# Optimization experiments

Measured on AMD Instinct MI355X. Metric: run time of the kernel, lower is better.

Reference implementation:

```python
import math
import jax, jax.numpy as jnp
import numpy as np

B, S, F, I, K, L, C = 2, 2048, 512, 1024, 3, 2, 256
BETA = 0.99                 # momentumnet_beta
INIT_SCALE = L ** -0.5      # per-cell output scale
PI = math.pi


def setup_inputs() -> dict:
    key = jax.random.key(0)
    ks = jax.random.split(key, 8)
    inp = jax.random.randint(ks[0], (B, S), 0, C)
    tgt = jax.random.randint(ks[1], (B, S), 0, C)
    emb = jax.random.normal(ks[2], (C, 2 * F), jnp.float32) * 0.02
    w0s = jax.random.normal(ks[3], (L, 3, I, F, 1), jnp.float32) * (F ** -0.5)
    w1s = jax.random.normal(ks[4], (L, 3, I, I, K), jnp.float32) * ((I * K) ** -0.5)
    w2s = jax.random.normal(ks[5], (L, 3, F, I, 1), jnp.float32) * (I ** -0.5)
    out_w = jax.random.normal(ks[6], (C, 2 * F, 1), jnp.float32) * ((2 * F) ** -0.5)
    out_b = jax.random.normal(ks[7], (C,), jnp.float32) * 0.02
    return {"inp": inp, "tgt": tgt, "emb": emb, "w0s": w0s, "w1s": w1s,
            "w2s": w2s, "out_w": out_w, "out_b": out_b}


def causal_conv(x, w):
    # x: [B, Cin, S], w: [Cout, Cin, k]; left-pad k-1 (matches torch pad+(k-1,0)+conv1d)
    k = w.shape[-1]
    return jax.lax.conv_general_dilated(x, w, (1,), [(k - 1, 0)],
                                        dimension_numbers=("NCH", "OIH", "NCH"))


def feed_forward(x, w0, w1, w2):
    x = jax.nn.relu(causal_conv(x, w0))
    x = jax.nn.relu(causal_conv(x, w1))
    return causal_conv(x, w2)


def norm(x):
    # mean-subtract + RMS-style L2 norm over channel dim (dim 1)
    x = x - x.mean(1, keepdims=True)
    return x / (jnp.linalg.norm(x, axis=1, keepdims=True) * (x.shape[1] ** -0.5) + 1e-5)


def _feature_embd():
    f = jnp.arange(F, dtype=jnp.float32)[:, None] + 1.0
    additive = f % 2.0
    f = (f - additive) / 2.0
    f = f * (8.0 / F) - math.log(C / (2.0 * PI))
    return jnp.exp(f) + additive * PI  # [F, 1]


def _forward(inp, tgt, emb, w0s, w1s, w2s, out_w, out_b):
    fe = _feature_embd()
    divisor = (jnp.arange(S, dtype=jnp.float32) + 1.0)[None, None, :]  # [1,1,S]
    x = emb[inp].transpose(0, 2, 1)         # [B, 2F, S]
    a, b = x[:, :F], x[:, F:]               # reversible streams [B, F, S]
    for l in range(L):
        h = b + fe                          # training-path positional embedding
        d = feed_forward(h, w0s[l, 0], w1s[l, 0], w2s[l, 0])
        sc = feed_forward(h, w0s[l, 1], w1s[l, 1], w2s[l, 1])
        sh = feed_forward(h, w0s[l, 2], w1s[l, 2], w2s[l, 2])
        cum = jnp.cumsum(d, axis=1)         # cumsum over feature dim (dim 1, as in source)
        cell = norm(cum / divisor * sc + sh) * INIT_SCALE
        c = BETA * a + (1.0 - BETA) * cell  # momentum coupling forward
        a, b = c, b + c                     # Identity layer with additive coupling
    streams = jnp.concatenate([a, b], axis=1)        # [B, 2F, S]
    logits = causal_conv(streams, out_w) + out_b[None, :, None]  # [B, C, S]
    logp = jax.nn.log_softmax(logits, axis=1)
    nll = -jnp.take_along_axis(logp, tgt[:, None, :], axis=1)[:, 0, :]
    return nll.mean()                       # torch cross_entropy (mean reduction)


def reference(inp, tgt, emb, w0s, w1s, w2s, out_w, out_b):
    return _forward(inp, tgt, emb, w0s, w1s, w2s, out_w, out_b)
```

## Files before the change

kernel.cpp:

```cpp
#include <hip/hip_runtime.h>

#define S_ 2048
#define F_ 512
#define I_ 1024
#define C_ 256

typedef float f4 __attribute__((ext_vector_type(4)));
typedef __bf16 bf8 __attribute__((ext_vector_type(8)));
typedef __bf16 bf4 __attribute__((ext_vector_type(4)));
typedef int i4v __attribute__((ext_vector_type(4)));
typedef int i8v __attribute__((ext_vector_type(8)));
typedef unsigned char u8;

__device__ __forceinline__ void gload_lds16(const void* g, void* l) {
  __builtin_amdgcn_global_load_lds(
      (const __attribute__((address_space(1))) void*)g,
      (__attribute__((address_space(3))) void*)l, 16, 0, 0);
}

__device__ __forceinline__ float fe_val(int f) {
  const float PI_F = 3.14159265358979323846f;
  float additive = (f & 1) ? 0.0f : 1.0f;
  float fv = ((float)(f + 1) - additive) * 0.5f;
  fv = fv * (8.0f / (float)F_) - logf((float)C_ / (2.0f * PI_F));
  return expf(fv) + additive * PI_F;
}

template <int KW, bool RELU, int OUT, int NTILE, int KD, int LDB>
__global__ __launch_bounds__(256) void gemm_f8(
    const u8* __restrict__ Ab, const u8* __restrict__ Bb, void* __restrict__ Cb,
    const u8* __restrict__ zpage, int M, int PZ, long sAp, long sBp, long sBb,
    long sCz) {
  constexpr int NF = NTILE / 32;
  constexpr int NIT = KD / 128;
  constexpr int AK = KW * KD;
  constexpr int BP = NTILE / 32;
  constexpr int NSTEP = KW * NIT;
  __shared__ u8 Asm[128 * 128];
  __shared__ u8 Bsm[NTILE * 128];
  const int tid = threadIdx.x;
  const int z = blockIdx.z;
  const int p = z % PZ;
  const int bb = z / PZ;
  const u8* A = Ab + (long)p * sAp;
  const u8* B = Bb + (long)bb * sBb + (long)p * sBp;
  const int m0 = blockIdx.y * 128;
  const int n0 = blockIdx.x * NTILE;
  const int lane = tid & 63;
  const int wave = tid >> 6;
  const int wr = wave >> 1;
  const int wc = wave & 1;
  const int l15 = lane & 15;
  const int quad = lane >> 4;
  const int cr = tid >> 3;
  const int csw = (((tid & 7) ^ (cr & 7)) << 4);
  const int off0 = (((2 * quad) ^ (l15 & 7)) << 4);
  const int off1 = (((2 * quad + 1) ^ (l15 & 7)) << 4);
  f4 acc[4][NF] = {};

  const int lin = blockIdx.x + gridDim.x * (blockIdx.y + gridDim.y * blockIdx.z);
  const int koff = ((lin >> 8) % 3) * (NSTEP / 3);

  auto kstep = [&](int ks) {
    const int t = (KW == 1) ? 0 : (ks / NIT);
    const int kb = (ks & (NIT - 1)) * 128;
    const u8* pA = A + (long)t * KD + kb;
#pragma unroll
    for (int g = 0; g < 4; ++g)
      gload_lds16(pA + (long)(m0 + g * 32 + cr) * AK + csw,
                  Asm + g * 4096 + wave * 1024);
#pragma unroll
    for (int g = 0; g < BP; ++g) {
      const int rg = n0 + g * 32 + cr + ((KW == 3) ? (t - 2) : 0);
      const u8* pB = (KW == 3 && rg < 0) ? (zpage + csw)
                                         : (B + (long)rg * LDB + kb + csw);
      gload_lds16(pB, Bsm + g * 4096 + wave * 1024);
    }
    __syncthreads();
    i8v af[4], bfr[NF];
#pragma unroll
    for (int mt = 0; mt < 4; ++mt) {
      const u8* rp = Asm + (wr * 64 + mt * 16 + l15) * 128;
      const i4v lo = *(const i4v*)(rp + off0);
      const i4v hi = *(const i4v*)(rp + off1);
      af[mt][0] = lo[0]; af[mt][1] = lo[1]; af[mt][2] = lo[2]; af[mt][3] = lo[3];
      af[mt][4] = hi[0]; af[mt][5] = hi[1]; af[mt][6] = hi[2]; af[mt][7] = hi[3];
    }
#pragma unroll
    for (int nt = 0; nt < NF; ++nt) {
      const u8* rp = Bsm + (wc * (NTILE / 2) + nt * 16 + l15) * 128;
      const i4v lo = *(const i4v*)(rp + off0);
      const i4v hi = *(const i4v*)(rp + off1);
      bfr[nt][0] = lo[0]; bfr[nt][1] = lo[1]; bfr[nt][2] = lo[2]; bfr[nt][3] = lo[3];
      bfr[nt][4] = hi[0]; bfr[nt][5] = hi[1]; bfr[nt][6] = hi[2]; bfr[nt][7] = hi[3];
    }
    __builtin_amdgcn_s_setprio(1);
#pragma unroll
    for (int mt = 0; mt < 4; ++mt)
#pragma unroll
      for (int nt = 0; nt < NF; ++nt)
        acc[mt][nt] = __builtin_amdgcn_mfma_scale_f32_16x16x128_f8f6f4(
            af[mt], bfr[nt], acc[mt][nt], 0, 0, 0, 0x7F7F7F7F, 0, 0x7F7F7F7F);
    __builtin_amdgcn_s_setprio(0);
    __syncthreads();
  };

#pragma unroll 1
  for (int ks = koff; ks < NSTEP; ++ks) kstep(ks);
#pragma unroll 1
  for (int ks = 0; ks < koff; ++ks) kstep(ks);

#pragma unroll
  for (int mt = 0; mt < 4; ++mt) {
    const int m = m0 + wr * 64 + mt * 16 + quad * 4;
#pragma unroll
    for (int nt = 0; nt < NF; ++nt) {
      const int n = n0 + wc * (NTILE / 2) + nt * 16 + l15;
      f4 v = acc[mt][nt];
#pragma unroll
      for (int q = 0; q < 4; ++q) {
        v[q] *= 0.015625f;
        if (RELU) v[q] = fmaxf(v[q], 0.0f);
      }
      if (OUT == 2) {
        int r = __builtin_amdgcn_cvt_pk_fp8_f32(v[0], v[1], 0, false);
        r = __builtin_amdgcn_cvt_pk_fp8_f32(v[2], v[3], r, true);
        *(int*)((u8*)Cb + (long)z * sCz + (long)n * M + m) = r;
      } else {
        *(f4*)((float*)Cb + (long)z * sCz + (long)n * M + m) = v;
      }
    }
  }
}

__device__ __forceinline__ void cvt4(const float* __restrict__ s,
                                     __bf16* __restrict__ d, long T) {
  const long i = T * 4;
  const float4 v = *(const float4*)(s + i);
  bf4 o;
  o[0] = (__bf16)v.x;
  o[1] = (__bf16)v.y;
  o[2] = (__bf16)v.z;
  o[3] = (__bf16)v.w;
  *(bf4*)(d + i) = o;
}

__device__ __forceinline__ void cvt4f8(const float* __restrict__ s,
                                       u8* __restrict__ d, long T) {
  const long i = T * 4;
  const float4 v = *(const float4*)(s + i);
  int r = __builtin_amdgcn_cvt_pk_fp8_f32(v.x * 64.0f, v.y * 64.0f, 0, false);
  r = __builtin_amdgcn_cvt_pk_fp8_f32(v.z * 64.0f, v.w * 64.0f, r, true);
  *(int*)(d + i) = r;
}

__device__ __forceinline__ int pk4f8(float a, float b, float c, float d) {
  int r = __builtin_amdgcn_cvt_pk_fp8_f32(a, b, 0, false);
  return __builtin_amdgcn_cvt_pk_fp8_f32(c, d, r, true);
}

__global__ void k_prep(const float* __restrict__ w0, const float* __restrict__ w2,
                       const float* __restrict__ ow, const float* __restrict__ w1,
                       u8* __restrict__ W0f8, u8* __restrict__ W2f8,
                       __bf16* __restrict__ OWc, u8* __restrict__ W1f8) {
  long T = (long)blockIdx.x * 256 + threadIdx.x;
  if (T < 786432L) {
    cvt4f8(w0, W0f8, T);
    return;
  }
  T -= 786432L;
  if (T < 786432L) {
    cvt4f8(w2, W2f8, T);
    return;
  }
  T -= 786432L;
  if (T < 65536L) {
    cvt4(ow, OWc, T);
    return;
  }
  T -= 65536L;
  const long j4 = T & 255;
  const long r3 = T >> 8;
  const float* src = w1 + r3 * 3072 + j4 * 12;
  const float4 v0 = *(const float4*)src;
  const float4 v1 = *(const float4*)(src + 4);
  const float4 v2 = *(const float4*)(src + 8);
  u8* dst = W1f8 + r3 * 3072 + j4 * 4;
  *(int*)(dst) = pk4f8(v0.x * 64.f, v0.w * 64.f, v1.z * 64.f, v2.y * 64.f);
  *(int*)(dst + 1024) = pk4f8(v0.y * 64.f, v1.x * 64.f, v1.w * 64.f, v2.z * 64.f);
  *(int*)(dst + 2048) = pk4f8(v0.z * 64.f, v1.y * 64.f, v2.x * 64.f, v2.w * 64.f);
}

__global__ __launch_bounds__(64) void k_embed(const int* __restrict__ inp,
                                              const float* __restrict__ emb,
                                              float* __restrict__ a_st,
                                              float* __restrict__ b_st,
                                              u8* __restrict__ h) {
  const int col = blockIdx.x;
  const int lane = threadIdx.x;
  const int f0 = lane * 8;
  const float* e = emb + (long)inp[col] * (2 * F_);
  const float4 a0 = *(const float4*)(e + f0);
  const float4 a1 = *(const float4*)(e + f0 + 4);
  const float4 b0 = *(const float4*)(e + F_ + f0);
  const float4 b1 = *(const float4*)(e + F_ + f0 + 4);
  *(float4*)(a_st + (long)col * F_ + f0) = a0;
  *(float4*)(a_st + (long)col * F_ + f0 + 4) = a1;
  *(float4*)(b_st + (long)col * F_ + f0) = b0;
  *(float4*)(b_st + (long)col * F_ + f0 + 4) = b1;
  const float bb[8] = {b0.x, b0.y, b0.z, b0.w, b1.x, b1.y, b1.z, b1.w};
  float hv[8];
#pragma unroll
  for (int q = 0; q < 8; ++q) hv[q] = bb[q] + fe_val(f0 + q);
  const int lo = pk4f8(hv[0], hv[1], hv[2], hv[3]);
  const int hi = pk4f8(hv[4], hv[5], hv[6], hv[7]);
  *(int2*)(h + (long)col * F_ + f0) = {lo, hi};
}

__global__ __launch_bounds__(64) void k_cell(const float* __restrict__ Y3,
                                             float* __restrict__ a_st,
                                             float* __restrict__ b_st,
                                             void* __restrict__ outp,
                                             int last) {
  const int col = blockIdx.x;
  const int s = col & (S_ - 1);
  const int b = col >> 11;
  const int lane = threadIdx.x;
  const int f0 = lane * 8;
  const float* d = Y3 + ((long)(3 * b + 0) * S_ + s) * F_ + f0;
  const float* sc = Y3 + ((long)(3 * b + 1) * S_ + s) * F_ + f0;
  const float* sh = Y3 + ((long)(3 * b + 2) * S_ + s) * F_ + f0;
  float* ap = a_st + (long)col * F_ + f0;
  float* bp = b_st + (long)col * F_ + f0;
  const float inv_div = 1.0f / (float)(s + 1);

  const float4 d0 = *(const float4*)d;
  const float4 d1 = *(const float4*)(d + 4);
  const float4 sc0 = *(const float4*)sc;
  const float4 sc1 = *(const float4*)(sc + 4);
  const float4 sh0 = *(const float4*)sh;
  const float4 sh1 = *(const float4*)(sh + 4);

  float c[8];
  c[0] = d0.x;
  c[1] = c[0] + d0.y;
  c[2] = c[1] + d0.z;
  c[3] = c[2] + d0.w;
  c[4] = c[3] + d1.x;
  c[5] = c[4] + d1.y;
  c[6] = c[5] + d1.z;
  c[7] = c[6] + d1.w;
  const float tot = c[7];
  float scan = tot;
#pragma unroll
  for (int off = 1; off < 64; off <<= 1) {
    float nb = __shfl_up(scan, off);
    if (lane >= off) scan += nb;
  }
  const float base = scan - tot;

  float v[8];
  v[0] = (base + c[0]) * inv_div * sc0.x + sh0.x;
  v[1] = (base + c[1]) * inv_div * sc0.y + sh0.y;
  v[2] = (base + c[2]) * inv_div * sc0.z + sh0.z;
  v[3] = (base + c[3]) * inv_div * sc0.w + sh0.w;
  v[4] = (base + c[4]) * inv_div * sc1.x + sh1.x;
  v[5] = (base + c[5]) * inv_div * sc1.y + sh1.y;
  v[6] = (base + c[6]) * inv_div * sc1.z + sh1.z;
  v[7] = (base + c[7]) * inv_div * sc1.w + sh1.w;

  float sum = 0.f, ssq = 0.f;
#pragma unroll
  for (int q = 0; q < 8; ++q) {
    sum += v[q];
    ssq += v[q] * v[q];
  }
#pragma unroll
  for (int off = 1; off < 64; off <<= 1) {
    sum += __shfl_xor(sum, off);
    ssq += __shfl_xor(ssq, off);
  }
  const float mean = sum * (1.0f / (float)F_);
  const float nsq = fmaxf(ssq - (float)F_ * mean * mean, 0.0f);
  const float denom = sqrtf(nsq) * 0.04419417382415922f + 1e-5f;
  const float isc = 0.7071067811865476f / denom;

  const float4 av0 = *(const float4*)ap;
  const float4 av1 = *(const float4*)(ap + 4);
  const float4 bv0 = *(const float4*)bp;
  const float4 bv1 = *(const float4*)(bp + 4);
  float an[8], bn[8];
  const float ai[8] = {av0.x, av0.y, av0.z, av0.w, av1.x, av1.y, av1.z, av1.w};
  const float bi[8] = {bv0.x, bv0.y, bv0.z, bv0.w, bv1.x, bv1.y, bv1.z, bv1.w};
#pragma unroll
  for (int q = 0; q < 8; ++q) {
    const float cell = (v[q] - mean) * isc;
    an[q] = 0.99f * ai[q] + 0.01f * cell;
    bn[q] = bi[q] + an[q];
  }
  *(float4*)ap = {an[0], an[1], an[2], an[3]};
  *(float4*)(ap + 4) = {an[4], an[5], an[6], an[7]};
  *(float4*)bp = {bn[0], bn[1], bn[2], bn[3]};
  *(float4*)(bp + 4) = {bn[4], bn[5], bn[6], bn[7]};
  if (!last) {
    float hv[8];
#pragma unroll
    for (int q = 0; q < 8; ++q) hv[q] = bn[q] + fe_val(f0 + q);
    const int lo = pk4f8(hv[0], hv[1], hv[2], hv[3]);
    const int hi = pk4f8(hv[4], hv[5], hv[6], hv[7]);
    *(int2*)((u8*)outp + (long)col * F_ + f0) = {lo, hi};
  } else {
    bf8 oa, ob;
#pragma unroll
    for (int q = 0; q < 8; ++q) {
      oa[q] = (__bf16)an[q];
      ob[q] = (__bf16)bn[q];
    }
    *(bf8*)((__bf16*)outp + (long)col * (2 * F_) + f0) = oa;
    *(bf8*)((__bf16*)outp + (long)col * (2 * F_) + F_ + f0) = ob;
  }
}

__global__ __launch_bounds__(256) void k_logits_nll(
    const __bf16* __restrict__ A, const __bf16* __restrict__ Bb,
    const float* __restrict__ outb, const int* __restrict__ tgt,
    float* __restrict__ acc) {
  __shared__ __bf16 As[256 * 32];
  __shared__ __bf16 Bs[32 * 32];
  __shared__ float lsm[32 * 256];
  const int tid = threadIdx.x;
  const int b = blockIdx.y;
  const int n0 = blockIdx.x * 32;
  const __bf16* Bt = Bb + (long)b * (S_ * 2 * F_) + (long)n0 * (2 * F_);
  const int lane = tid & 63;
  const int wave = tid >> 6;
  const int l15 = lane & 15;
  const int quad = lane >> 4;
  const int cr = tid >> 2;
  const int csw = (((tid & 3) ^ ((cr >> 1) & 3)) << 3);
  const int roff = ((quad ^ ((l15 >> 1) & 3)) << 3);
  f4 av[4][2] = {};
  for (int k0 = 0; k0 < 2 * F_; k0 += 32) {
#pragma unroll
    for (int i = 0; i < 4; ++i)
      gload_lds16(A + (long)(i * 64 + cr) * (2 * F_) + (k0 + csw),
                  As + ((i * 256 + (wave << 6)) << 3));
    if (wave < 2)
      gload_lds16(Bt + (long)cr * (2 * F_) + (k0 + csw),
                  Bs + ((wave << 6) << 3));
    __syncthreads();
    bf8 af[4], bfr[2];
#pragma unroll
    for (int mt = 0; mt < 4; ++mt)
      af[mt] = *(const bf8*)(As + (wave * 64 + mt * 16 + l15) * 32 + roff);
#pragma unroll
    for (int nt = 0; nt < 2; ++nt)
      bfr[nt] = *(const bf8*)(Bs + (nt * 16 + l15) * 32 + roff);
#pragma unroll
    for (int mt = 0; mt < 4; ++mt)
#pragma unroll
      for (int nt = 0; nt < 2; ++nt)
        av[mt][nt] = __builtin_amdgcn_mfma_f32_16x16x32_bf16(af[mt], bfr[nt],
                                                             av[mt][nt], 0, 0, 0);
    __syncthreads();
  }
#pragma unroll
  for (int mt = 0; mt < 4; ++mt) {
    const int m = wave * 64 + mt * 16 + quad * 4;
#pragma unroll
    for (int nt = 0; nt < 2; ++nt) {
      const int pp = nt * 16 + l15;
      *(f4*)(lsm + pp * C_ + m) = av[mt][nt];
    }
  }
  __syncthreads();
  const float4 bv = *(const float4*)(outb + lane * 4);
  float wsum = 0.f;
  for (int i = 0; i < 8; ++i) {
    const int pp = wave * 8 + i;
    const f4 lv = *(const f4*)(lsm + pp * C_ + lane * 4);
    const float x0 = lv[0] + bv.x, x1 = lv[1] + bv.y, x2 = lv[2] + bv.z,
                x3 = lv[3] + bv.w;
    float mx = fmaxf(fmaxf(x0, x1), fmaxf(x2, x3));
#pragma unroll
    for (int off = 1; off < 64; off <<= 1) mx = fmaxf(mx, __shfl_xor(mx, off));
    float ss = expf(x0 - mx) + expf(x1 - mx) + expf(x2 - mx) + expf(x3 - mx);
#pragma unroll
    for (int off = 1; off < 64; off <<= 1) ss += __shfl_xor(ss, off);
    if (lane == 0) {
      const int t = tgt[b * S_ + n0 + pp];
      wsum += mx + logf(ss) - (lsm[pp * C_ + t] + outb[t]);
    }
  }
  if (lane == 0) atomicAdd(acc, wsum);
}

__global__ void k_final(const float* __restrict__ acc, float* __restrict__ out) {
  out[0] = acc[0] * (1.0f / 4096.0f);
}

extern "C" void kernel_launch(void* const* d_in, const int* in_sizes, int n_in,
                              void* d_out, int out_size, void* d_ws,
                              size_t ws_size, hipStream_t stream) {
  const int* inp = (const int*)d_in[0];
  const int* tgt = (const int*)d_in[1];
  const float* emb = (const float*)d_in[2];
  const float* w0s = (const float*)d_in[3];
  const float* w1s = (const float*)d_in[4];
  const float* w2s = (const float*)d_in[5];
  const float* out_w = (const float*)d_in[6];
  const float* out_b = (const float*)d_in[7];

  char* ws = (char*)d_ws;
  float* acc = (float*)(ws + 0);
  u8* zp = (u8*)(ws + 256);
  float* a_st = (float*)(ws + 4096);
  float* b_st = (float*)(ws + 8392704L);
  u8* h = (u8*)(ws + 16781312L);
  u8* Y1f8 = (u8*)(ws + 20975616L);
  u8* Y2f8 = (u8*)(ws + 46141440L);
  float* Y3 = (float*)(ws + 71307264L);
  u8* W1f8 = (u8*)(ws + 96473088L);
  __bf16* streams = (__bf16*)(ws + 134221824L);
  u8* W0f8 = (u8*)(ws + 146804736L);
  u8* W2f8 = (u8*)(ws + 153096192L);
  __bf16* OWc = (__bf16*)(ws + 159387648L);

  hipMemsetAsync(ws, 0, 4096, stream);
  k_prep<<<12544, 256, 0, stream>>>(w0s, w2s, out_w, w1s, W0f8, W2f8, OWc, W1f8);
  k_embed<<<4096, 64, 0, stream>>>(inp, emb, a_st, b_st, h);

  for (int l = 0; l < 2; ++l) {
    gemm_f8<1, true, 2, 128, 512, 512><<<dim3(16, 24, 2), 256, 0, stream>>>(
        W0f8 + (long)l * 1572864L, h, Y1f8, zp, 3072, 1, 0L, 0L, 1048576L,
        6291456L);
    gemm_f8<3, true, 2, 128, 1024, 3072><<<dim3(16, 8, 6), 256, 0, stream>>>(
        W1f8 + (long)l * 9437184L, Y1f8, Y2f8, zp, 1024, 3, 3145728L, 1024L,
        6291456L, 2097152L);
    gemm_f8<1, false, 0, 64, 1024, 1024><<<dim3(32, 4, 6), 256, 0, stream>>>(
        W2f8 + (long)l * 1572864L, Y2f8, Y3, zp, 512, 3, 524288L, 2097152L,
        6291456L, 1048576L);
    k_cell<<<4096, 64, 0, stream>>>(Y3, a_st, b_st,
                                    (l == 0) ? (void*)h : (void*)streams,
                                    (l == 1) ? 1 : 0);
  }

  k_logits_nll<<<dim3(64, 2), 256, 0, stream>>>(OWc, streams, out_b, tgt, acc);
  k_final<<<1, 1, 0, stream>>>(acc, (float*)d_out);
}
```

Before: 366.4 us.

## Double-buffer B tile in LDS and load A fragments directly to registers

```diff
diff --git a/kernel.cpp b/kernel.cpp
--- a/kernel.cpp
+++ b/kernel.cpp
@@ -27,7 +27,7 @@
 }
 
 template <int KW, bool RELU, int OUT, int NTILE, int KD, int LDB>
-__global__ __launch_bounds__(256) void gemm_f8(
+__global__ __launch_bounds__(256, 3) void gemm_f8(
     const u8* __restrict__ Ab, const u8* __restrict__ Bb, void* __restrict__ Cb,
     const u8* __restrict__ zpage, int M, int PZ, long sAp, long sBp, long sBb,
     long sCz) {
@@ -36,8 +36,8 @@
   constexpr int AK = KW * KD;
   constexpr int BP = NTILE / 32;
   constexpr int NSTEP = KW * NIT;
-  __shared__ u8 Asm[128 * 128];
-  __shared__ u8 Bsm[NTILE * 128];
+  static_assert(NSTEP % 2 == 0, "even k-step count required");
+  __shared__ u8 Bsm[2][NTILE * 128];
   const int tid = threadIdx.x;
   const int z = blockIdx.z;
   const int p = z % PZ;
@@ -58,37 +58,40 @@
   const int off1 = (((2 * quad + 1) ^ (l15 & 7)) << 4);
   f4 acc[4][NF] = {};
 
-  const int lin = blockIdx.x + gridDim.x * (blockIdx.y + gridDim.y * blockIdx.z);
-  const int koff = ((lin >> 8) % 3) * (NSTEP / 3);
-
-  auto kstep = [&](int ks) {
+  const u8* Arow[4];
+#pragma unroll
+  for (int mt = 0; mt < 4; ++mt)
+    Arow[mt] = A + (long)(m0 + wr * 64 + mt * 16 + l15) * AK + quad * 32;
+
+  auto loadA = [&](int ks, i8v* ar) {
+    const int t = (KW == 1) ? 0 : (ks / NIT);
+    const long o = (long)t * KD + (ks & (NIT - 1)) * 128;
+#pragma unroll
+    for (int mt = 0; mt < 4; ++mt) {
+      const i4v lo = *(const i4v*)(Arow[mt] + o);
+      const i4v hi = *(const i4v*)(Arow[mt] + o + 16);
+      ar[mt][0] = lo[0]; ar[mt][1] = lo[1]; ar[mt][2] = lo[2]; ar[mt][3] = lo[3];
+      ar[mt][4] = hi[0]; ar[mt][5] = hi[1]; ar[mt][6] = hi[2]; ar[mt][7] = hi[3];
+    }
+  };
+
+  auto stageB = [&](int ks, int buf) {
     const int t = (KW == 1) ? 0 : (ks / NIT);
     const int kb = (ks & (NIT - 1)) * 128;
-    const u8* pA = A + (long)t * KD + kb;
-#pragma unroll
-    for (int g = 0; g < 4; ++g)
-      gload_lds16(pA + (long)(m0 + g * 32 + cr) * AK + csw,
-                  Asm + g * 4096 + wave * 1024);
 #pragma unroll
     for (int g = 0; g < BP; ++g) {
       const int rg = n0 + g * 32 + cr + ((KW == 3) ? (t - 2) : 0);
       const u8* pB = (KW == 3 && rg < 0) ? (zpage + csw)
                                          : (B + (long)rg * LDB + kb + csw);
-      gload_lds16(pB, Bsm + g * 4096 + wave * 1024);
-    }
-    __syncthreads();
-    i8v af[4], bfr[NF];
-#pragma unroll
-    for (int mt = 0; mt < 4; ++mt) {
-      const u8* rp = Asm + (wr * 64 + mt * 16 + l15) * 128;
-      const i4v lo = *(const i4v*)(rp + off0);
-      const i4v hi = *(const i4v*)(rp + off1);
-      af[mt][0] = lo[0]; af[mt][1] = lo[1]; af[mt][2] = lo[2]; af[mt][3] = lo[3];
-      af[mt][4] = hi[0]; af[mt][5] = hi[1]; af[mt][6] = hi[2]; af[mt][7] = hi[3];
-    }
+      gload_lds16(pB, &Bsm[buf][g * 4096 + wave * 1024]);
+    }
+  };
+
+  auto compute = [&](const i8v* ar, int buf) {
+    i8v bfr[NF];
 #pragma unroll
     for (int nt = 0; nt < NF; ++nt) {
-      const u8* rp = Bsm + (wc * (NTILE / 2) + nt * 16 + l15) * 128;
+      const u8* rp = &Bsm[buf][(wc * (NTILE / 2) + nt * 16 + l15) * 128];
       const i4v lo = *(const i4v*)(rp + off0);
       const i4v hi = *(const i4v*)(rp + off1);
       bfr[nt][0] = lo[0]; bfr[nt][1] = lo[1]; bfr[nt][2] = lo[2]; bfr[nt][3] = lo[3];
@@ -100,15 +103,25 @@
 #pragma unroll
       for (int nt = 0; nt < NF; ++nt)
         acc[mt][nt] = __builtin_amdgcn_mfma_scale_f32_16x16x128_f8f6f4(
-            af[mt], bfr[nt], acc[mt][nt], 0, 0, 0, 0x7F7F7F7F, 0, 0x7F7F7F7F);
+            ar[mt], bfr[nt], acc[mt][nt], 0, 0, 0, 0x7F7F7F7F, 0, 0x7F7F7F7F);
     __builtin_amdgcn_s_setprio(0);
+  };
+
+  i8v aA[4];
+  loadA(0, aA);
+  stageB(0, 0);
+  __syncthreads();
+#pragma unroll 1
+  for (int ks = 0; ks < NSTEP; ks += 2) {
+    stageB(ks + 1, 1);
+    compute(aA, 0);
+    loadA(ks + 1, aA);
     __syncthreads();
-  };
-
-#pragma unroll 1
-  for (int ks = koff; ks < NSTEP; ++ks) kstep(ks);
-#pragma unroll 1
-  for (int ks = 0; ks < koff; ++ks) kstep(ks);
+    if (ks + 2 < NSTEP) stageB(ks + 2, 0);
+    compute(aA, 1);
+    if (ks + 2 < NSTEP) loadA(ks + 2, aA);
+    __syncthreads();
+  }
 
 #pragma unroll
   for (int mt = 0; mt < 4; ++mt) {
```

Result: slower. 1.049 ms (+186.4%).

## Double-buffer the B tile in the FP8 GEMM k-loop and drop the k-offset rotation

Applied to the files above, without the earlier changes.

```diff
diff --git a/kernel.cpp b/kernel.cpp
--- a/kernel.cpp
+++ b/kernel.cpp
@@ -36,8 +36,9 @@
   constexpr int AK = KW * KD;
   constexpr int BP = NTILE / 32;
   constexpr int NSTEP = KW * NIT;
+  static_assert(NSTEP % 2 == 0, "even k-step count required");
   __shared__ u8 Asm[128 * 128];
-  __shared__ u8 Bsm[NTILE * 128];
+  __shared__ u8 Bsm[2][NTILE * 128];
   const int tid = threadIdx.x;
   const int z = blockIdx.z;
   const int p = z % PZ;
@@ -58,10 +59,7 @@
   const int off1 = (((2 * quad + 1) ^ (l15 & 7)) << 4);
   f4 acc[4][NF] = {};
 
-  const int lin = blockIdx.x + gridDim.x * (blockIdx.y + gridDim.y * blockIdx.z);
-  const int koff = ((lin >> 8) % 3) * (NSTEP / 3);
-
-  auto kstep = [&](int ks) {
+  auto stageA = [&](int ks) {
     const int t = (KW == 1) ? 0 : (ks / NIT);
     const int kb = (ks & (NIT - 1)) * 128;
     const u8* pA = A + (long)t * KD + kb;
@@ -69,14 +67,21 @@
     for (int g = 0; g < 4; ++g)
       gload_lds16(pA + (long)(m0 + g * 32 + cr) * AK + csw,
                   Asm + g * 4096 + wave * 1024);
+  };
+
+  auto stageB = [&](int ks, int buf) {
+    const int t = (KW == 1) ? 0 : (ks / NIT);
+    const int kb = (ks & (NIT - 1)) * 128;
 #pragma unroll
     for (int g = 0; g < BP; ++g) {
       const int rg = n0 + g * 32 + cr + ((KW == 3) ? (t - 2) : 0);
       const u8* pB = (KW == 3 && rg < 0) ? (zpage + csw)
                                          : (B + (long)rg * LDB + kb + csw);
-      gload_lds16(pB, Bsm + g * 4096 + wave * 1024);
-    }
-    __syncthreads();
+      gload_lds16(pB, &Bsm[buf][g * 4096 + wave * 1024]);
+    }
+  };
+
+  auto compute = [&](int buf) {
     i8v af[4], bfr[NF];
 #pragma unroll
     for (int mt = 0; mt < 4; ++mt) {
@@ -88,7 +93,7 @@
     }
 #pragma unroll
     for (int nt = 0; nt < NF; ++nt) {
-      const u8* rp = Bsm + (wc * (NTILE / 2) + nt * 16 + l15) * 128;
+      const u8* rp = &Bsm[buf][(wc * (NTILE / 2) + nt * 16 + l15) * 128];
       const i4v lo = *(const i4v*)(rp + off0);
       const i4v hi = *(const i4v*)(rp + off1);
       bfr[nt][0] = lo[0]; bfr[nt][1] = lo[1]; bfr[nt][2] = lo[2]; bfr[nt][3] = lo[3];
@@ -102,13 +107,26 @@
         acc[mt][nt] = __builtin_amdgcn_mfma_scale_f32_16x16x128_f8f6f4(
             af[mt], bfr[nt], acc[mt][nt], 0, 0, 0, 0x7F7F7F7F, 0, 0x7F7F7F7F);
     __builtin_amdgcn_s_setprio(0);
+  };
+
+  stageA(0);
+  stageB(0, 0);
+  __syncthreads();
+#pragma unroll 1
+  for (int ks = 0; ks < NSTEP; ks += 2) {
+    stageB(ks + 1, 1);
+    compute(0);
     __syncthreads();
-  };
-
-#pragma unroll 1
-  for (int ks = koff; ks < NSTEP; ++ks) kstep(ks);
-#pragma unroll 1
-  for (int ks = 0; ks < koff; ++ks) kstep(ks);
+    stageA(ks + 1);
+    __syncthreads();
+    if (ks + 2 < NSTEP) stageB(ks + 2, 0);
+    compute(1);
+    if (ks + 2 < NSTEP) {
+      __syncthreads();
+      stageA(ks + 2);
+      __syncthreads();
+    }
+  }
 
 #pragma unroll
   for (int mt = 0; mt < 4; ++mt) {
```

Result: slower. 414.0 us (+13.0%).

## Reuse B tile across conv taps via rotating LDS row buffer

Applied to the files above, without the earlier changes.

```diff
diff --git a/kernel.cpp b/kernel.cpp
--- a/kernel.cpp
+++ b/kernel.cpp
@@ -58,25 +58,33 @@
   const int off1 = (((2 * quad + 1) ^ (l15 & 7)) << 4);
   f4 acc[4][NF] = {};
 
-  const int lin = blockIdx.x + gridDim.x * (blockIdx.y + gridDim.y * blockIdx.z);
-  const int koff = ((lin >> 8) % 3) * (NSTEP / 3);
-
-  auto kstep = [&](int ks) {
-    const int t = (KW == 1) ? 0 : (ks / NIT);
-    const int kb = (ks & (NIT - 1)) * 128;
-    const u8* pA = A + (long)t * KD + kb;
+  auto stageA = [&](int t, int kb) {
+    const u8* pA = A + (long)t * KD + kb * 128;
 #pragma unroll
     for (int g = 0; g < 4; ++g)
       gload_lds16(pA + (long)(m0 + g * 32 + cr) * AK + csw,
                   Asm + g * 4096 + wave * 1024);
+  };
+
+  auto stageBfull = [&](int t, int kb) {
 #pragma unroll
     for (int g = 0; g < BP; ++g) {
       const int rg = n0 + g * 32 + cr + ((KW == 3) ? (t - 2) : 0);
       const u8* pB = (KW == 3 && rg < 0) ? (zpage + csw)
-                                         : (B + (long)rg * LDB + kb + csw);
+                                         : (B + (long)rg * LDB + kb * 128 + csw);
       gload_lds16(pB, Bsm + g * 4096 + wave * 1024);
     }
-    __syncthreads();
+  };
+
+  auto stageBrow = [&](int hrow, int kb) {
+    if (wave == 0 && lane < 8) {
+      const u8* pB =
+          B + (long)(n0 + 126 + hrow) * LDB + kb * 128 + ((lane ^ hrow) << 4);
+      gload_lds16(pB, Bsm + hrow * 128);
+    }
+  };
+
+  auto computeB = [&](int tshift) {
     i8v af[4], bfr[NF];
 #pragma unroll
     for (int mt = 0; mt < 4; ++mt) {
@@ -86,29 +94,55 @@
       af[mt][0] = lo[0]; af[mt][1] = lo[1]; af[mt][2] = lo[2]; af[mt][3] = lo[3];
       af[mt][4] = hi[0]; af[mt][5] = hi[1]; af[mt][6] = hi[2]; af[mt][7] = hi[3];
     }
+    const int bkey = ((l15 + tshift) & 7);
+    const int bo0 = (((2 * quad) ^ bkey) << 4);
+    const int bo1 = (((2 * quad + 1) ^ bkey) << 4);
 #pragma unroll
     for (int nt = 0; nt < NF; ++nt) {
-      const u8* rp = Bsm + (wc * (NTILE / 2) + nt * 16 + l15) * 128;
-      const i4v lo = *(const i4v*)(rp + off0);
-      const i4v hi = *(const i4v*)(rp + off1);
+      const int hr = (wc * (NTILE / 2) + nt * 16 + l15 + tshift) & (NTILE - 1);
+      const u8* rp = Bsm + hr * 128;
+      const i4v lo = *(const i4v*)(rp + bo0);
+      const i4v hi = *(const i4v*)(rp + bo1);
       bfr[nt][0] = lo[0]; bfr[nt][1] = lo[1]; bfr[nt][2] = lo[2]; bfr[nt][3] = lo[3];
       bfr[nt][4] = hi[0]; bfr[nt][5] = hi[1]; bfr[nt][6] = hi[2]; bfr[nt][7] = hi[3];
     }
-    __builtin_amdgcn_s_setprio(1);
 #pragma unroll
     for (int mt = 0; mt < 4; ++mt)
 #pragma unroll
       for (int nt = 0; nt < NF; ++nt)
         acc[mt][nt] = __builtin_amdgcn_mfma_scale_f32_16x16x128_f8f6f4(
             af[mt], bfr[nt], acc[mt][nt], 0, 0, 0, 0x7F7F7F7F, 0, 0x7F7F7F7F);
-    __builtin_amdgcn_s_setprio(0);
-    __syncthreads();
   };
 
+  if constexpr (KW == 1) {
 #pragma unroll 1
-  for (int ks = koff; ks < NSTEP; ++ks) kstep(ks);
+    for (int ks = 0; ks < NSTEP; ++ks) {
+      stageA(0, ks);
+      stageBfull(0, ks);
+      __syncthreads();
+      computeB(0);
+      __syncthreads();
+    }
+  } else {
 #pragma unroll 1
-  for (int ks = 0; ks < koff; ++ks) kstep(ks);
+    for (int kb = 0; kb < NIT; ++kb) {
+      stageA(0, kb);
+      stageBfull(0, kb);
+      __syncthreads();
+      computeB(0);
+      __syncthreads();
+      stageA(1, kb);
+      stageBrow(0, kb);
+      __syncthreads();
+      computeB(1);
+      __syncthreads();
+      stageA(2, kb);
+      stageBrow(1, kb);
+      __syncthreads();
+      computeB(2);
+      __syncthreads();
+    }
+  }
 
 #pragma unroll
   for (int mt = 0; mt < 4; ++mt) {
```

After: 376.3 us. 2.7% more time.
